# Kernel tuning notes

Measured on AMD Instinct MI355X. Metric: run time of the kernel, lower is better.

The kernel has to match this reference:

```python
import jax, jax.numpy as jnp
import numpy as np

B, L, D_MODEL, HEAD, DK = 4, 4096, 1024, 8, 128
ROUNDS, BUCKET = 4, 64
N_BUCKETS = L // BUCKET  # number of hash buckets AND number of chunks
NEG, SELF_PEN, EPS = -1e9, -1e5, 1e-5


def setup_inputs() -> dict:
    key = jax.random.key(0)
    ks = jax.random.split(key, 9)
    s = 0.02
    rot = jax.random.normal(ks[5], (DK, ROUNDS, N_BUCKETS // 2), dtype=jnp.float32)
    rot = rot / (jnp.linalg.norm(rot, axis=0, keepdims=True) + 1e-9)  # unit-norm rotations
    return {
        'x1': jax.random.normal(ks[0], (B, L, D_MODEL), jnp.float32),
        'x2': jax.random.normal(ks[1], (B, L, D_MODEL), jnp.float32),
        'wq': jax.random.normal(ks[2], (D_MODEL, D_MODEL), jnp.float32) * s,
        'bq': jnp.zeros((D_MODEL,), jnp.float32),
        'wv': jax.random.normal(ks[3], (D_MODEL, D_MODEL), jnp.float32) * s,
        'bv': jnp.zeros((D_MODEL,), jnp.float32),
        'wo': jax.random.normal(ks[4], (D_MODEL, D_MODEL), jnp.float32) * s,
        'bo': jnp.zeros((D_MODEL,), jnp.float32),
        'gamma': jnp.ones((D_MODEL,), jnp.float32),
        'beta': jnp.zeros((D_MODEL,), jnp.float32),
        'rot': rot,
        'mask': jnp.ones((B, L), jnp.bool_),
    }


def _look_back(t):
    # concat previous chunk (circular) with current chunk along intra-chunk axis
    prev = jnp.roll(t, 1, axis=3)
    return jnp.concatenate([prev, t], axis=4)


def _lsh_attention(x, mask, wq, bq, wv, bv, wo, bo, rot):
    # x: [B, L, D]; mask: [B, L] bool; rot: [DK, R, N_BUCKETS//2]
    q = (x @ wq + bq).reshape(B, L, HEAD, DK).transpose(0, 2, 1, 3)  # [B,H,L,dk]
    v = (x @ wv + bv).reshape(B, L, HEAD, DK).transpose(0, 2, 1, 3)
    # LSH hashing: argmax over [proj, -proj]
    proj = jnp.einsum('bhld,drn->bhrln', q, rot)  # [B,H,R,L,nb/2]
    hashes = jnp.argmax(jnp.concatenate([proj, -proj], axis=-1), axis=-1)  # [B,H,R,L]
    pos = jnp.arange(L)
    sort_idx = jnp.argsort(hashes * L + pos[None, None, None, :], axis=-1)  # stable sort by hash
    undo_idx = jnp.argsort(sort_idx, axis=-1)
    # gather q, v, positions, mask into hash-sorted order per round
    sq = jnp.take_along_axis(jnp.broadcast_to(q[:, :, None], (B, HEAD, ROUNDS, L, DK)), sort_idx[..., None], axis=3)
    sv = jnp.take_along_axis(jnp.broadcast_to(v[:, :, None], (B, HEAD, ROUNDS, L, DK)), sort_idx[..., None], axis=3)
    spos = jnp.take_along_axis(jnp.broadcast_to(pos, (B, HEAD, ROUNDS, L)), sort_idx, axis=3)
    smask = jnp.take_along_axis(jnp.broadcast_to(mask[:, None, None, :], (B, HEAD, ROUNDS, L)), sort_idx, axis=3)
    nc = L // BUCKET
    sq = sq.reshape(B, HEAD, ROUNDS, nc, BUCKET, DK)
    sv = sv.reshape(B, HEAD, ROUNDS, nc, BUCKET, DK)
    spos = spos.reshape(B, HEAD, ROUNDS, nc, BUCKET)
    smask = smask.reshape(B, HEAD, ROUNDS, nc, BUCKET)
    # shared-QK: keys are L2-normalized queries
    sk = sq / (jnp.linalg.norm(sq, axis=-1, keepdims=True) + 1e-9)
    k_lb, v_lb = _look_back(sk), _look_back(sv)          # [B,H,R,nc,2*BUCKET,dk]
    kpos, kmask = _look_back(spos[..., None]).squeeze(-1) if False else (_look_back(spos[..., None])[..., 0], _look_back(smask[..., None])[..., 0])
    scores = jnp.einsum('bhrcid,bhrcjd->bhrcij', sq, k_lb) / np.float32(np.sqrt(DK))
    qp = spos[..., :, None]
    kp = kpos[..., None, :]
    scores = jnp.where(kmask[..., None, :], scores, NEG)      # padding
    scores = jnp.where(kp > qp, NEG, scores)                  # causal
    scores = jnp.where(kp == qp, SELF_PEN, scores)            # discourage self-attention
    attn = jax.nn.softmax(scores, axis=-1)
    lse = jax.nn.logsumexp(scores, axis=-1)                   # [B,H,R,nc,BUCKET]
    o = jnp.einsum('bhrcij,bhrcjd->bhrcid', attn, v_lb).reshape(B, HEAD, ROUNDS, L, DK)
    lse = lse.reshape(B, HEAD, ROUNDS, L)
    # unsort back to original order
    o = jnp.take_along_axis(o, undo_idx[..., None], axis=3)
    lse = jnp.take_along_axis(lse, undo_idx, axis=3)
    # combine rounds with softmax over per-round logsumexp
    w = jax.nn.softmax(lse, axis=2)[..., None]                # [B,H,R,L,1]
    out = (w * o).sum(axis=2)                                 # [B,H,L,dk]
    out = out.transpose(0, 2, 1, 3).reshape(B, L, D_MODEL)
    return out @ wo + bo


def _layernorm(x, g, b):
    mu = jnp.mean(x, axis=-1, keepdims=True)
    var = jnp.mean((x - mu) ** 2, axis=-1, keepdims=True)
    return (x - mu) / jnp.sqrt(var + EPS) * g + b


def reference(x1, x2, wq, bq, wv, bv, wo, bo, gamma, beta, rot, mask):
    a = _lsh_attention(x2, mask, wq, bq, wv, bv, wo, bo, rot)
    y1 = x1 + _layernorm(a, gamma, beta)  # dropout is identity in eval
    return (y1, x2)
```

## Files before the change

kernel.cpp:

```cpp
#include <hip/hip_runtime.h>
#include <hip/hip_bf16.h>

#define B_ 4
#define L_ 4096
#define DM_ 1024
#define NH_ 8
#define DK_ 128
#define NR_ 4
#define NC_ 64
#define NEGV -1.0e9f
#define SELFP -1.0e5f
#define SQRTDK 11.313708498984761f
#define TAU 1.0e-3f
#define FCAP 524288
#define LOG2E 1.4426950408889634f
#define LN2 0.6931471805599453f

typedef __attribute__((ext_vector_type(8))) short short8;
typedef __attribute__((ext_vector_type(4))) float f32x4;

__device__ __forceinline__ unsigned short f2bf(float x) {
  unsigned u = __float_as_uint(x);
  u += 0x7FFFu + ((u >> 16) & 1u);
  return (unsigned short)(u >> 16);
}
__device__ __forceinline__ float bf2f(unsigned short h) {
  return __uint_as_float(((unsigned)h) << 16);
}
__device__ __forceinline__ float wlo(unsigned w) { return __uint_as_float(w << 16); }
__device__ __forceinline__ float whi(unsigned w) { return __uint_as_float(w & 0xFFFF0000u); }
__device__ __forceinline__ unsigned packbf(float a, float b) {
  unsigned r;
  asm("v_cvt_pk_bf16_f32 %0, %1, %2" : "=v"(r) : "v"(a), "v"(b));
  return r;
}
__device__ __forceinline__ float fexp2(float x) {
  float r;
  asm("v_exp_f32 %0, %1" : "=v"(r) : "v"(x));
  return r;
}
__device__ __forceinline__ float flog2(float x) {
  float r;
  asm("v_log_f32 %0, %1" : "=v"(r) : "v"(x));
  return r;
}
__device__ __forceinline__ unsigned packhi(float a, float b) {
  return (__float_as_uint(a) >> 16) | (__float_as_uint(b) & 0xFFFF0000u);
}
__device__ __forceinline__ float resid(float a) {
  return a - __uint_as_float(__float_as_uint(a) & 0xFFFF0000u);
}

__global__ __launch_bounds__(256) void cvtw_k(const float* __restrict__ W,
                                              unsigned short* __restrict__ Wt) {
  __shared__ float tile[64][65];
  const int t = threadIdx.x;
  const int bx = blockIdx.x & 15, by = blockIdx.x >> 4;
  const int c = t & 63, r4 = t >> 6;
#pragma unroll
  for (int i = 0; i < 16; i++) {
    int r = r4 * 16 + i;
    tile[r][c] = W[(size_t)(by * 64 + r) * DM_ + bx * 64 + c];
  }
  __syncthreads();
#pragma unroll
  for (int i = 0; i < 16; i++) {
    int r = r4 * 16 + i;
    Wt[(size_t)(bx * 64 + r) * DM_ + by * 64 + c] = f2bf(tile[c][r]);
  }
}

__global__ __launch_bounds__(256) void cvtw2_k(const float* __restrict__ W,
                                               unsigned short* __restrict__ Whi,
                                               unsigned short* __restrict__ Wlo) {
  __shared__ float tile[64][65];
  const int t = threadIdx.x;
  const int bx = blockIdx.x & 15, by = blockIdx.x >> 4;
  const int c = t & 63, r4 = t >> 6;
#pragma unroll
  for (int i = 0; i < 16; i++) {
    int r = r4 * 16 + i;
    tile[r][c] = W[(size_t)(by * 64 + r) * DM_ + bx * 64 + c];
  }
  __syncthreads();
#pragma unroll
  for (int i = 0; i < 16; i++) {
    int r = r4 * 16 + i;
    float v = tile[c][r];
    unsigned short h = f2bf(v);
    float lo = v - bf2f(h);
    size_t o = (size_t)(bx * 64 + r) * DM_ + by * 64 + c;
    Whi[o] = h;
    Wlo[o] = f2bf(lo);
  }
}

__global__ __launch_bounds__(256) void cvtrot_k(const float* __restrict__ rot,
                                                unsigned short* __restrict__ Rhi,
                                                unsigned short* __restrict__ Rlo) {
  int i = blockIdx.x * 256 + threadIdx.x;
  float v = rot[i];
  unsigned short h = f2bf(v);
  float lo = v - bf2f(h);
  int d = i >> 7, np = i & 127;
  Rhi[np * 128 + d] = h;
  Rlo[np * 128 + d] = f2bf(lo);
}

__global__ __launch_bounds__(256) void wproj_k(const float* __restrict__ W,
                                               const float* __restrict__ rot,
                                               float* __restrict__ Wp,
                                               int* __restrict__ cnt) {
  __shared__ float ws_[8][128];
  __shared__ float rs[128][33];
  const int t = threadIdx.x;
  const int hr = blockIdx.x >> 7;
  const int kc = blockIdx.x & 127;
  const int h = hr >> 2, r = hr & 3;
  if (blockIdx.x == 0 && t == 0) *cnt = 0;
  for (int i = t; i < 4096; i += 256) {
    int d = i >> 5, n = i & 31;
    rs[d][n] = rot[(size_t)d * 128 + r * 32 + n];
  }
  {
    int kk = t >> 5, dd = (t & 31) * 4;
    const float* wr = W + (size_t)(kc * 8 + kk) * DM_ + h * 128 + dd;
    float4 wv = *(const float4*)wr;
    ws_[kk][dd] = wv.x; ws_[kk][dd + 1] = wv.y;
    ws_[kk][dd + 2] = wv.z; ws_[kk][dd + 3] = wv.w;
  }
  __syncthreads();
  const int n = t & 31, kk = t >> 5;
  float s0 = 0.f, s1 = 0.f, s2 = 0.f, s3 = 0.f;
#pragma unroll
  for (int d = 0; d < 128; d += 4) {
    s0 = fmaf(ws_[kk][d], rs[d][n], s0);
    s1 = fmaf(ws_[kk][d + 1], rs[d + 1][n], s1);
    s2 = fmaf(ws_[kk][d + 2], rs[d + 2][n], s2);
    s3 = fmaf(ws_[kk][d + 3], rs[d + 3][n], s3);
  }
  Wp[((size_t)(h * 4 + r) * 32 + n) * 1024 + kc * 8 + kk] = (s0 + s1) + (s2 + s3);
}

__global__ __launch_bounds__(256) void gemm_qs(const unsigned short* __restrict__ Whi,
                                               const unsigned short* __restrict__ Wlo,
                                               const float* __restrict__ X,
                                               const float* __restrict__ bias,
                                               float* __restrict__ outF) {
  __shared__ __align__(16) unsigned short Ph[128 * 32];
  __shared__ __align__(16) unsigned short Pl[128 * 32];
  __shared__ __align__(16) unsigned short Qh[128 * 32];
  __shared__ __align__(16) unsigned short Ql[128 * 32];
  __shared__ float bias_s[128];
  const int t = threadIdx.x;
  const int bi = blockIdx.x;
  const int pb = (bi & 7) << 7;
  const int qb = (bi >> 3) << 7;
  if (t < 128) bias_s[t] = bias[pb + t];
  const int srow = t >> 1, shalf = t & 1;
  const unsigned short* Ph_p = Whi + (size_t)(pb + srow) * DM_ + shalf * 16;
  const unsigned short* Pl_p = Wlo + (size_t)(pb + srow) * DM_ + shalf * 16;
  const float* Xf = X + (size_t)(qb + srow) * DM_ + shalf * 16;
  const int lane = t & 63, wid = t >> 6;
  const int lm = lane & 15, quad = lane >> 4;
  const int prw = (wid & 1) << 6, qcw = (wid >> 1) << 6;
  const int sg = (quad ^ (lm & 3)) << 3;
  f32x4 acc[4][4];
#pragma unroll
  for (int i = 0; i < 4; i++)
#pragma unroll
    for (int j = 0; j < 4; j++) acc[i][j] = (f32x4){0.f, 0.f, 0.f, 0.f};
  uint4 phA, phB, plA, plB, qhA, qhB, qlA, qlB;
  {
    phA = *(const uint4*)(Ph_p);
    phB = *(const uint4*)(Ph_p + 8);
    plA = *(const uint4*)(Pl_p);
    plB = *(const uint4*)(Pl_p + 8);
    float4 f0 = *(const float4*)(Xf), f1 = *(const float4*)(Xf + 4);
    float4 f2 = *(const float4*)(Xf + 8), f3 = *(const float4*)(Xf + 12);
    qhA.x = packhi(f0.x, f0.y); qhA.y = packhi(f0.z, f0.w);
    qhA.z = packhi(f1.x, f1.y); qhA.w = packhi(f1.z, f1.w);
    qhB.x = packhi(f2.x, f2.y); qhB.y = packhi(f2.z, f2.w);
    qhB.z = packhi(f3.x, f3.y); qhB.w = packhi(f3.z, f3.w);
    qlA.x = packbf(resid(f0.x), resid(f0.y)); qlA.y = packbf(resid(f0.z), resid(f0.w));
    qlA.z = packbf(resid(f1.x), resid(f1.y)); qlA.w = packbf(resid(f1.z), resid(f1.w));
    qlB.x = packbf(resid(f2.x), resid(f2.y)); qlB.y = packbf(resid(f2.z), resid(f2.w));
    qlB.z = packbf(resid(f3.x), resid(f3.y)); qlB.w = packbf(resid(f3.z), resid(f3.w));
  }
  const int sw = srow & 3, g0 = shalf * 2;
  const int d0s = srow * 32 + ((g0 ^ sw) << 3);
  const int d1s = srow * 32 + (((g0 + 1) ^ sw) << 3);
  for (int kb = 0; kb < 32; ++kb) {
    __syncthreads();
    *(uint4*)&Ph[d0s] = phA; *(uint4*)&Ph[d1s] = phB;
    *(uint4*)&Pl[d0s] = plA; *(uint4*)&Pl[d1s] = plB;
    *(uint4*)&Qh[d0s] = qhA; *(uint4*)&Qh[d1s] = qhB;
    *(uint4*)&Ql[d0s] = qlA; *(uint4*)&Ql[d1s] = qlB;
    __syncthreads();
    if (kb < 31) {
      int ko = (kb + 1) * 32;
      phA = *(const uint4*)(Ph_p + ko);
      phB = *(const uint4*)(Ph_p + ko + 8);
      plA = *(const uint4*)(Pl_p + ko);
      plB = *(const uint4*)(Pl_p + ko + 8);
      const float* xp = Xf + ko;
      float4 f0 = *(const float4*)(xp), f1 = *(const float4*)(xp + 4);
      float4 f2 = *(const float4*)(xp + 8), f3 = *(const float4*)(xp + 12);
      qhA.x = packhi(f0.x, f0.y); qhA.y = packhi(f0.z, f0.w);
      qhA.z = packhi(f1.x, f1.y); qhA.w = packhi(f1.z, f1.w);
      qhB.x = packhi(f2.x, f2.y); qhB.y = packhi(f2.z, f2.w);
      qhB.z = packhi(f3.x, f3.y); qhB.w = packhi(f3.z, f3.w);
      qlA.x = packbf(resid(f0.x), resid(f0.y)); qlA.y = packbf(resid(f0.z), resid(f0.w));
      qlA.z = packbf(resid(f1.x), resid(f1.y)); qlA.w = packbf(resid(f1.z), resid(f1.w));
      qlB.x = packbf(resid(f2.x), resid(f2.y)); qlB.y = packbf(resid(f2.z), resid(f2.w));
      qlB.z = packbf(resid(f3.x), resid(f3.y)); qlB.w = packbf(resid(f3.z), resid(f3.w));
    }
    short8 ph[4], pl[4], qh[4], ql[4];
#pragma unroll
    for (int ti = 0; ti < 4; ti++) {
      int ro = (prw + ti * 16 + lm) * 32 + sg;
      ph[ti] = *(const short8*)&Ph[ro];
      pl[ti] = *(const short8*)&Pl[ro];
    }
#pragma unroll
    for (int tj = 0; tj < 4; tj++) {
      int ro = (qcw + tj * 16 + lm) * 32 + sg;
      qh[tj] = *(const short8*)&Qh[ro];
      ql[tj] = *(const short8*)&Ql[ro];
    }
#pragma unroll
    for (int ti = 0; ti < 4; ti++)
#pragma unroll
      for (int tj = 0; tj < 4; tj++) {
        f32x4 a = acc[ti][tj];
        a = __builtin_amdgcn_mfma_f32_16x16x32_bf16(ph[ti], qh[tj], a, 0, 0, 0);
        a = __builtin_amdgcn_mfma_f32_16x16x32_bf16(ph[ti], ql[tj], a, 0, 0, 0);
        a = __builtin_amdgcn_mfma_f32_16x16x32_bf16(pl[ti], qh[tj], a, 0, 0, 0);
        acc[ti][tj] = a;
      }
  }
  const int head = bi & 7;
#pragma unroll
  for (int tj = 0; tj < 4; tj++) {
    int mm = qb + qcw + tj * 16 + lm;
    int b = mm >> 12, l = mm & 4095;
    float* op = outF + ((size_t)(b * NH_ + head) * L_ + l) * DK_;
#pragma unroll
    for (int ti = 0; ti < 4; ti++) {
      int d0 = prw + ti * 16 + quad * 4;
      float4 w;
      w.x = acc[ti][tj][0] + bias_s[d0];
      w.y = acc[ti][tj][1] + bias_s[d0 + 1];
      w.z = acc[ti][tj][2] + bias_s[d0 + 2];
      w.w = acc[ti][tj][3] + bias_s[d0 + 3];
      *(float4*)(op + d0) = w;
    }
  }
}

template <int MODE>
__global__ __launch_bounds__(256) void gemm_bf(const unsigned short* __restrict__ Pm,
                                               const void* __restrict__ Qv,
                                               const float* __restrict__ bias,
                                               float* __restrict__ outF,
                                               unsigned int* __restrict__ outW) {
  __shared__ __align__(16) unsigned short Ps[128 * 32];
  __shared__ __align__(16) unsigned short Qs[128 * 32];
  __shared__ float bias_s[128];
  const int t = threadIdx.x;
  const int bi = blockIdx.x;
  const int pb = (MODE == 0) ? ((bi >> 3) << 7) : ((bi & 7) << 7);
  const int qb = (MODE == 0) ? ((bi & 7) << 7) : ((bi >> 3) << 7);
  if (t < 128) bias_s[t] = bias[((MODE == 0) ? qb : pb) + t];
  const int srow = t >> 1, shalf = t & 1;
  const unsigned short* Pp = Pm + (size_t)(pb + srow) * DM_ + shalf * 16;
  const float* Qf = (const float*)Qv + (size_t)(qb + srow) * DM_ + shalf * 16;
  const unsigned short* Qh = (const unsigned short*)Qv + (size_t)(qb + srow) * DM_ + shalf * 16;
  const int lane = t & 63, wid = t >> 6;
  const int lm = lane & 15, quad = lane >> 4;
  const int prw = (wid & 1) << 6, qcw = (wid >> 1) << 6;
  f32x4 acc[4][4];
#pragma unroll
  for (int i = 0; i < 4; i++)
#pragma unroll
    for (int j = 0; j < 4; j++) acc[i][j] = (f32x4){0.f, 0.f, 0.f, 0.f};
  uint4 pA, pB, qA, qB;
  {
    pA = *(const uint4*)(Pp);
    pB = *(const uint4*)(Pp + 8);
    if (MODE == 2) {
      float4 f0 = *(const float4*)(Qf), f1 = *(const float4*)(Qf + 4);
      float4 f2 = *(const float4*)(Qf + 8), f3 = *(const float4*)(Qf + 12);
      qA.x = packbf(f0.x, f0.y); qA.y = packbf(f0.z, f0.w);
      qA.z = packbf(f1.x, f1.y); qA.w = packbf(f1.z, f1.w);
      qB.x = packbf(f2.x, f2.y); qB.y = packbf(f2.z, f2.w);
      qB.z = packbf(f3.x, f3.y); qB.w = packbf(f3.z, f3.w);
    } else {
      qA = *(const uint4*)(Qh);
      qB = *(const uint4*)(Qh + 8);
    }
  }
  const int sdst = srow * 32 + shalf * 16;
  for (int kb = 0; kb < 32; ++kb) {
    __syncthreads();
    *(uint4*)&Ps[sdst] = pA;
    *(uint4*)&Ps[sdst + 8] = pB;
    *(uint4*)&Qs[sdst] = qA;
    *(uint4*)&Qs[sdst + 8] = qB;
    __syncthreads();
    if (kb < 31) {
      int ko = (kb + 1) * 32;
      pA = *(const uint4*)(Pp + ko);
      pB = *(const uint4*)(Pp + ko + 8);
      if (MODE == 2) {
        const float* qp = Qf + ko;
        float4 f0 = *(const float4*)(qp), f1 = *(const float4*)(qp + 4);
        float4 f2 = *(const float4*)(qp + 8), f3 = *(const float4*)(qp + 12);
        qA.x = packbf(f0.x, f0.y); qA.y = packbf(f0.z, f0.w);
        qA.z = packbf(f1.x, f1.y); qA.w = packbf(f1.z, f1.w);
        qB.x = packbf(f2.x, f2.y); qB.y = packbf(f2.z, f2.w);
        qB.z = packbf(f3.x, f3.y); qB.w = packbf(f3.z, f3.w);
      } else {
        qA = *(const uint4*)(Qh + ko);
        qB = *(const uint4*)(Qh + ko + 8);
      }
    }
    short8 pf[4], qf[4];
#pragma unroll
    for (int ti = 0; ti < 4; ti++)
      pf[ti] = *(const short8*)&Ps[(prw + ti * 16 + lm) * 32 + quad * 8];
#pragma unroll
    for (int tj = 0; tj < 4; tj++)
      qf[tj] = *(const short8*)&Qs[(qcw + tj * 16 + lm) * 32 + quad * 8];
#pragma unroll
    for (int ti = 0; ti < 4; ti++)
#pragma unroll
      for (int tj = 0; tj < 4; tj++)
        acc[ti][tj] = __builtin_amdgcn_mfma_f32_16x16x32_bf16(pf[ti], qf[tj], acc[ti][tj], 0, 0, 0);
  }
  if (MODE == 0) {
#pragma unroll
    for (int ti = 0; ti < 4; ti++) {
      int m = pb + prw + ti * 16 + quad * 4;
#pragma unroll
      for (int tj = 0; tj < 4; tj++) {
        int nn = qcw + tj * 16 + lm;
        float bn = bias_s[nn];
        float* op = outF + (size_t)m * DM_ + qb + nn;
#pragma unroll
        for (int r = 0; r < 4; r++) op[(size_t)r * DM_] = acc[ti][tj][r] + bn;
      }
    }
  } else {
    const int head = bi & 7;
#pragma unroll
    for (int tj = 0; tj < 4; tj++) {
      int mm = qb + qcw + tj * 16 + lm;
      int b = mm >> 12, l = mm & 4095;
#pragma unroll
      for (int ti = 0; ti < 4; ti++) {
        int d0 = prw + ti * 16 + quad * 4;
        uint2 ov;
        ov.x = packbf(acc[ti][tj][0] + bias_s[d0], acc[ti][tj][1] + bias_s[d0 + 1]);
        ov.y = packbf(acc[ti][tj][2] + bias_s[d0 + 2], acc[ti][tj][3] + bias_s[d0 + 3]);
        *(uint2*)(outW + ((size_t)(b * NH_ + head) * L_ + l) * 64 + (d0 >> 1)) = ov;
      }
    }
  }
}

#define HSTR 132
__global__ __launch_bounds__(256) void hashg_k(const unsigned short* __restrict__ Rhi,
                                               const unsigned short* __restrict__ Rlo,
                                               const float* __restrict__ q,
                                               unsigned char* __restrict__ hout,
                                               int* __restrict__ cnt,
                                               int* __restrict__ flags) {
  __shared__ __align__(16) char smraw[128 * HSTR * 4];
  unsigned short* Ph = (unsigned short*)smraw;
  unsigned short* Pl = Ph + 4096;
  unsigned short* Qh = Ph + 8192;
  unsigned short* Ql = Ph + 12288;
  float* S = (float*)smraw;
  const int t = threadIdx.x;
  const int bi = blockIdx.x;
  const int srow = t >> 1, shalf = t & 1;
  const unsigned short* Php = Rhi + srow * 128 + shalf * 16;
  const unsigned short* Plp = Rlo + srow * 128 + shalf * 16;
  const float* Qf = q + (size_t)(bi * 128 + srow) * DK_ + shalf * 16;
  const int lane = t & 63, wid = t >> 6;
  const int lm = lane & 15, quad = lane >> 4;
  const int prw = (wid & 1) << 6, qcw = (wid >> 1) << 6;
  const int sg = (quad ^ (lm & 3)) << 3;
  f32x4 acc[4][4];
#pragma unroll
  for (int i = 0; i < 4; i++)
#pragma unroll
    for (int j = 0; j < 4; j++) acc[i][j] = (f32x4){0.f, 0.f, 0.f, 0.f};
  const int sw = srow & 3, g0 = shalf * 2;
  const int d0s = srow * 32 + ((g0 ^ sw) << 3);
  const int d1s = srow * 32 + (((g0 + 1) ^ sw) << 3);
  for (int kb = 0; kb < 4; ++kb) {
    const int ko = kb * 32;
    uint4 phA = *(const uint4*)(Php + ko);
    uint4 phB = *(const uint4*)(Php + ko + 8);
    uint4 plA = *(const uint4*)(Plp + ko);
    uint4 plB = *(const uint4*)(Plp + ko + 8);
    const float* xp = Qf + ko;
    float4 f0 = *(const float4*)(xp), f1 = *(const float4*)(xp + 4);
    float4 f2 = *(const float4*)(xp + 8), f3 = *(const float4*)(xp + 12);
    uint4 qhA, qhB, qlA, qlB;
    qhA.x = packhi(f0.x, f0.y); qhA.y = packhi(f0.z, f0.w);
    qhA.z = packhi(f1.x, f1.y); qhA.w = packhi(f1.z, f1.w);
    qhB.x = packhi(f2.x, f2.y); qhB.y = packhi(f2.z, f2.w);
    qhB.z = packhi(f3.x, f3.y); qhB.w = packhi(f3.z, f3.w);
    qlA.x = packbf(resid(f0.x), resid(f0.y)); qlA.y = packbf(resid(f0.z), resid(f0.w));
    qlA.z = packbf(resid(f1.x), resid(f1.y)); qlA.w = packbf(resid(f1.z), resid(f1.w));
    qlB.x = packbf(resid(f2.x), resid(f2.y)); qlB.y = packbf(resid(f2.z), resid(f2.w));
    qlB.z = packbf(resid(f3.x), resid(f3.y)); qlB.w = packbf(resid(f3.z), resid(f3.w));
    __syncthreads();
    *(uint4*)&Ph[d0s] = phA; *(uint4*)&Ph[d1s] = phB;
    *(uint4*)&Pl[d0s] = plA; *(uint4*)&Pl[d1s] = plB;
    *(uint4*)&Qh[d0s] = qhA; *(uint4*)&Qh[d1s] = qhB;
    *(uint4*)&Ql[d0s] = qlA; *(uint4*)&Ql[d1s] = qlB;
    __syncthreads();
    short8 ph[4], pl[4], qh[4], ql[4];
#pragma unroll
    for (int ti = 0; ti < 4; ti++) {
      int ro = (prw + ti * 16 + lm) * 32 + sg;
      ph[ti] = *(const short8*)&Ph[ro];
      pl[ti] = *(const short8*)&Pl[ro];
    }
#pragma unroll
    for (int tj = 0; tj < 4; tj++) {
      int ro = (qcw + tj * 16 + lm) * 32 + sg;
      qh[tj] = *(const short8*)&Qh[ro];
      ql[tj] = *(const short8*)&Ql[ro];
    }
#pragma unroll
    for (int ti = 0; ti < 4; ti++)
#pragma unroll
      for (int tj = 0; tj < 4; tj++) {
        f32x4 a = acc[ti][tj];
        a = __builtin_amdgcn_mfma_f32_16x16x32_bf16(ph[ti], qh[tj], a, 0, 0, 0);
        a = __builtin_amdgcn_mfma_f32_16x16x32_bf16(ph[ti], ql[tj], a, 0, 0, 0);
        a = __builtin_amdgcn_mfma_f32_16x16x32_bf16(pl[ti], qh[tj], a, 0, 0, 0);
        acc[ti][tj] = a;
      }
  }
  __syncthreads();
#pragma unroll
  for (int ti = 0; ti < 4; ti++)
#pragma unroll
    for (int tj = 0; tj < 4; tj++) {
      int nn = qcw + tj * 16 + lm;
#pragma unroll
      for (int r = 0; r < 4; r++)
        S[(prw + ti * 16 + quad * 4 + r) * HSTR + nn] = acc[ti][tj][r];
    }
  __syncthreads();
#pragma unroll
  for (int pp = t; pp < 512; pp += 256) {
    int tok = pp & 127, r = pp >> 7;
    float best = -1.f, second = -1.f;
    int bidx = 0;
#pragma unroll
    for (int n = 0; n < 32; n++) {
      float v = S[(r * 32 + n) * HSTR + tok];
      float av = fabsf(v);
      int idx = (v >= 0.f) ? n : (n + 32);
      if (av > best) {
        second = best; best = av; bidx = idx;
      } else {
        if (av == best && idx < bidx) bidx = idx;
        second = fmaxf(second, av);
      }
    }
    int mm = bi * 128 + tok;
    int bh = mm >> 12, l = mm & 4095;
    hout[((size_t)(bh * NR_ + r)) * L_ + l] = (unsigned char)bidx;
    if (best - second < TAU) {
      int slot = atomicAdd(cnt, 1);
      if (slot < FCAP) flags[slot] = (((bh << 2) | r) << 12) | l;
    }
  }
}

__global__ __launch_bounds__(256) void fixup_k(const int* __restrict__ cnt,
                                               const int* __restrict__ flags,
                                               const float* __restrict__ X,
                                               const float* __restrict__ Wp,
                                               unsigned char* __restrict__ hout) {
  __shared__ float xs[1024];
  __shared__ float pv[32];
  int nflag = *cnt;
  if (nflag > FCAP) nflag = FCAP;
  const int t = threadIdx.x;
  for (int i = blockIdx.x; i < nflag; i += gridDim.x) {
    int f = flags[i];
    int l = f & 4095, r = (f >> 12) & 3, bh = f >> 14;
    int b = bh >> 3, h = bh & 7;
    __syncthreads();
    ((float4*)xs)[t] = ((const float4*)(X + ((size_t)b * L_ + l) * DM_))[t];
    __syncthreads();
    const int nn = t >> 3, kl = t & 7;
    const float* wrow = Wp + ((size_t)(h * 4 + r) * 32 + nn) * 1024 + kl * 4;
    float s = 0.f;
#pragma unroll 8
    for (int k0 = 0; k0 < 1024; k0 += 32) {
      float4 wv = *(const float4*)(wrow + k0);
      float4 xv = *(const float4*)(xs + k0 + kl * 4);
      s = fmaf(wv.x, xv.x, fmaf(wv.y, xv.y, fmaf(wv.z, xv.z, fmaf(wv.w, xv.w, s))));
    }
    s += __shfl_xor(s, 1);
    s += __shfl_xor(s, 2);
    s += __shfl_xor(s, 4);
    if (kl == 0) pv[nn] = s;
    __syncthreads();
    if (t == 0) {
      float bestv = -1.f;
      int besti = 0;
      for (int j = 0; j < 32; j++) {
        float p = pv[j];
        float ap = fabsf(p);
        int idx = (p >= 0.f) ? j : (j + 32);
        if (ap > bestv || (ap == bestv && idx < besti)) { bestv = ap; besti = idx; }
      }
      hout[((size_t)(bh * NR_ + r)) * L_ + l] = (unsigned char)besti;
    }
  }
}

__global__ __launch_bounds__(256) void sort_k(const unsigned char* __restrict__ hsh,
                                              int* __restrict__ sidx) {
  __shared__ unsigned char seg[256 * 64];
  __shared__ unsigned short grp[16 * 64];
  __shared__ int offs[64];
  __shared__ int tot[64];
  const int t = threadIdx.x;
  const int bhr = blockIdx.x;
  uint4 hv = ((const uint4*)(hsh + (size_t)bhr * L_))[t];
  unsigned hb[4] = {hv.x, hv.y, hv.z, hv.w};
  unsigned int* seg32 = (unsigned int*)seg;
#pragma unroll
  for (int i = 0; i < 16; i++) seg32[t * 16 + i] = 0;
  ((unsigned int*)grp)[t * 2] = 0;
  ((unsigned int*)grp)[t * 2 + 1] = 0;
  __syncthreads();
#pragma unroll
  for (int k = 0; k < 16; k++) {
    int h = (hb[k >> 2] >> ((k & 3) * 8)) & 0xFF;
    seg[t * 64 + h] = (unsigned char)(seg[t * 64 + h] + 1);
  }
  __syncthreads();
  {
    int h = t & 63;
    for (int g = (t >> 6); g < 16; g += 4) {
      int run = 0;
      for (int s = 0; s < 16; s++) {
        int idx = ((g << 4) + s) * 64 + h;
        int c = seg[idx];
        seg[idx] = (unsigned char)run;
        run += c;
      }
      grp[g * 64 + h] = (unsigned short)run;
    }
  }
  __syncthreads();
  if (t < 64) {
    int run = 0;
    for (int g = 0; g < 16; g++) {
      int c = grp[g * 64 + t];
      grp[g * 64 + t] = (unsigned short)run;
      run += c;
    }
    tot[t] = run;
  }
  __syncthreads();
  if (t == 0) {
    int run = 0;
    for (int h = 0; h < 64; h++) { offs[h] = run; run += tot[h]; }
  }
  __syncthreads();
  const int gbase = (t >> 4) * 64;
  int* outp = sidx + (size_t)bhr * L_;
#pragma unroll
  for (int k = 0; k < 16; k++) {
    int h = (hb[k >> 2] >> ((k & 3) * 8)) & 0xFF;
    int pos = offs[h] + grp[gbase + h] + seg[t * 64 + h];
    seg[t * 64 + h] = (unsigned char)(seg[t * 64 + h] + 1);
    outp[pos] = t * 16 + k;
  }
}

#define KSTR 136
__global__ __launch_bounds__(256) void attn_k(const float* __restrict__ q,
                                              const unsigned int* __restrict__ vwg,
                                              const int* __restrict__ sidx,
                                              float* __restrict__ lseG,
                                              unsigned int* __restrict__ oW) {
  __shared__ __align__(16) unsigned short R1[128 * KSTR];
  __shared__ __align__(16) unsigned short R2[64 * KSTR];
  __shared__ int idxs[128];
  const int t = threadIdx.x;
  const int c = blockIdx.x & 63;
  const int bhr = blockIdx.x >> 6;
  const int bh = bhr >> 2;
  const int pc = (c + 63) & 63;
  if (t < 128) {
    int sp = (t < 64) ? (pc * 64 + t) : (c * 64 + t - 64);
    idxs[t] = sidx[(size_t)bhr * L_ + sp];
  }
  __syncthreads();
  {
    const int row = t >> 1, half = t & 1;
    const float4* qp = (const float4*)(q + ((size_t)bh * L_ + idxs[row]) * DK_ + half * 64);
    float4 f[16];
    float ss = 0.f;
#pragma unroll
    for (int u = 0; u < 16; u++) {
      f[u] = qp[u];
      ss = fmaf(f[u].x, f[u].x, fmaf(f[u].y, f[u].y, fmaf(f[u].z, f[u].z, fmaf(f[u].w, f[u].w, ss))));
    }
    ss += __shfl_xor(ss, 1);
    float rn = 1.f / (sqrtf(ss) + 1e-9f);
    unsigned short* kr = R1 + row * KSTR + half * 64;
#pragma unroll
    for (int u = 0; u < 8; u++) {
      uint4 w4;
      w4.x = packbf(f[2 * u].x * rn, f[2 * u].y * rn);
      w4.y = packbf(f[2 * u].z * rn, f[2 * u].w * rn);
      w4.z = packbf(f[2 * u + 1].x * rn, f[2 * u + 1].y * rn);
      w4.w = packbf(f[2 * u + 1].z * rn, f[2 * u + 1].w * rn);
      *(uint4*)(kr + u * 8) = w4;
    }
    if (row >= 64) {
      unsigned short* qr = R2 + (row - 64) * KSTR + half * 64;
#pragma unroll
      for (int u = 0; u < 8; u++) {
        uint4 w4;
        w4.x = packbf(f[2 * u].x, f[2 * u].y);
        w4.y = packbf(f[2 * u].z, f[2 * u].w);
        w4.z = packbf(f[2 * u + 1].x, f[2 * u + 1].y);
        w4.w = packbf(f[2 * u + 1].z, f[2 * u + 1].w);
        *(uint4*)(qr + u * 8) = w4;
      }
    }
  }
  __syncthreads();
  const int lane = t & 63, wv = t >> 6;
  const int m0 = wv * 16;
  const int lm = lane & 15, quad = lane >> 4;
  f32x4 acc[8];
  {
    short8 af[4];
#pragma unroll
    for (int ks = 0; ks < 4; ks++)
      af[ks] = *(const short8*)(R2 + (m0 + lm) * KSTR + ks * 32 + quad * 8);
#pragma unroll
    for (int n = 0; n < 8; n++) {
      f32x4 a = {0.f, 0.f, 0.f, 0.f};
#pragma unroll
      for (int ks = 0; ks < 4; ks++) {
        short8 bf = *(const short8*)(R1 + (n * 16 + lm) * KSTR + ks * 32 + quad * 8);
        a = __builtin_amdgcn_mfma_f32_16x16x32_bf16(af[ks], bf, a, 0, 0, 0);
      }
      acc[n] = a;
    }
  }
  int qp4[4];
#pragma unroll
  for (int r = 0; r < 4; r++) qp4[r] = idxs[64 + m0 + quad * 4 + r];
#pragma unroll
  for (int n = 0; n < 8; n++) {
    int kp = idxs[n * 16 + lm];
#pragma unroll
    for (int r = 0; r < 4; r++) {
      float s = acc[n][r] * (1.f / SQRTDK);
      acc[n][r] = (kp > qp4[r]) ? NEGV : ((kp == qp4[r]) ? SELFP : s);
    }
  }
  uint4 vv[8];
  {
    const int key = t >> 1, half = t & 1;
    const uint4* vp = (const uint4*)(vwg + ((size_t)bh * L_ + idxs[key]) * 64 + half * 32);
#pragma unroll
    for (int u = 0; u < 8; u++) vv[u] = vp[u];
  }
  float mrow[4], sum4[4], inv4[4];
#pragma unroll
  for (int r = 0; r < 4; r++) {
    float mx = acc[0][r];
#pragma unroll
    for (int n = 1; n < 8; n++) mx = fmaxf(mx, acc[n][r]);
    mx = fmaxf(mx, __shfl_xor(mx, 1));
    mx = fmaxf(mx, __shfl_xor(mx, 2));
    mx = fmaxf(mx, __shfl_xor(mx, 4));
    mx = fmaxf(mx, __shfl_xor(mx, 8));
    mrow[r] = mx;
    sum4[r] = 0.f;
  }
#pragma unroll
  for (int n = 0; n < 8; n++) {
#pragma unroll
    for (int r = 0; r < 4; r++) {
      float e = fexp2((acc[n][r] - mrow[r]) * LOG2E);
      unsigned pk = packbf(e, e);
      R2[(m0 + quad * 4 + r) * KSTR + n * 16 + lm] = (unsigned short)pk;
      sum4[r] += wlo(pk);
    }
  }
#pragma unroll
  for (int r = 0; r < 4; r++) {
    float s = sum4[r];
    s += __shfl_xor(s, 1);
    s += __shfl_xor(s, 2);
    s += __shfl_xor(s, 4);
    s += __shfl_xor(s, 8);
    sum4[r] = s;
    inv4[r] = 1.f / s;
  }
  if (lm == 0) {
#pragma unroll
    for (int r = 0; r < 4; r++)
      lseG[(size_t)bhr * L_ + idxs[64 + m0 + quad * 4 + r]] = mrow[r] + flog2(sum4[r]) * LN2;
  }
  __syncthreads();
  {
    const int key = t >> 1, half = t & 1;
#pragma unroll
    for (int u = 0; u < 8; u++) {
      unsigned wd[4] = {vv[u].x, vv[u].y, vv[u].z, vv[u].w};
#pragma unroll
      for (int cc = 0; cc < 4; cc++) {
        int w = half * 32 + u * 4 + cc;
        R1[(2 * w) * KSTR + key] = (unsigned short)(wd[cc] & 0xFFFFu);
        R1[(2 * w + 1) * KSTR + key] = (unsigned short)(wd[cc] >> 16);
      }
    }
  }
  __syncthreads();
  f32x4 acc2[8];
  {
    short8 af[4];
#pragma unroll
    for (int ks = 0; ks < 4; ks++)
      af[ks] = *(const short8*)(R2 + (m0 + lm) * KSTR + ks * 32 + quad * 8);
#pragma unroll
    for (int n = 0; n < 8; n++) {
      f32x4 a = {0.f, 0.f, 0.f, 0.f};
#pragma unroll
      for (int ks = 0; ks < 4; ks++) {
        short8 bf = *(const short8*)(R1 + (n * 16 + lm) * KSTR + ks * 32 + quad * 8);
        a = __builtin_amdgcn_mfma_f32_16x16x32_bf16(af[ks], bf, a, 0, 0, 0);
      }
      acc2[n] = a;
    }
  }
#pragma unroll
  for (int n = 0; n < 8; n++) {
#pragma unroll
    for (int r = 0; r < 4; r++) {
      float o = acc2[n][r] * inv4[r];
      R2[(m0 + quad * 4 + r) * KSTR + n * 16 + lm] = (unsigned short)packbf(o, o);
    }
  }
  __syncthreads();
  {
    const int row = t >> 2, seg = t & 3;
    int l = idxs[64 + row];
    unsigned int* op = oW + ((size_t)bhr * L_ + l) * 64 + seg * 16;
    const unsigned short* rp = R2 + row * KSTR + seg * 32;
#pragma unroll
    for (int u = 0; u < 4; u++) *(uint4*)(op + u * 4) = *(const uint4*)(rp + u * 8);
  }
}

__global__ __launch_bounds__(256) void comb_k(const float* __restrict__ lse,
                                              const unsigned int* __restrict__ oW,
                                              unsigned int* __restrict__ aoutW) {
  size_t g = (size_t)blockIdx.x * 256 + threadIdx.x;
  int w = (int)(g & 63);
  int l = (int)((g >> 6) & 4095);
  int bh = (int)(g >> 18);
  float ls[4];
#pragma unroll
  for (int r = 0; r < 4; r++) ls[r] = lse[((size_t)(bh * 4 + r)) * L_ + l];
  float m = fmaxf(fmaxf(ls[0], ls[1]), fmaxf(ls[2], ls[3]));
  float wsum = 0.f, a0 = 0.f, a1 = 0.f;
#pragma unroll
  for (int r = 0; r < 4; r++) {
    float e = fexp2((ls[r] - m) * LOG2E);
    wsum += e;
    unsigned ow = oW[(((size_t)(bh * 4 + r)) * L_ + l) * 64 + w];
    a0 = fmaf(e, wlo(ow), a0);
    a1 = fmaf(e, whi(ow), a1);
  }
  float inv = 1.f / wsum;
  int b = bh >> 3, h = bh & 7;
  aoutW[((size_t)b * L_ + l) * 512 + h * 64 + w] = packbf(a0 * inv, a1 * inv);
}

__global__ __launch_bounds__(256) void ln_k(const float* __restrict__ a,
                                            const float* __restrict__ x1,
                                            const float* __restrict__ x2,
                                            const float* __restrict__ gamma,
                                            const float* __restrict__ beta,
                                            float* __restrict__ out) {
  __shared__ float red[256];
  __shared__ float red2[256];
  const int t = threadIdx.x;
  const size_t row = blockIdx.x;
  float4 av = *(const float4*)(a + row * DM_ + t * 4);
  red[t] = av.x + av.y + av.z + av.w;
  red2[t] = av.x * av.x + av.y * av.y + av.z * av.z + av.w * av.w;
  __syncthreads();
  for (int off = 128; off > 0; off >>= 1) {
    if (t < off) { red[t] += red[t + off]; red2[t] += red2[t + off]; }
    __syncthreads();
  }
  float mu = red[0] * (1.f / 1024.f);
  float var = red2[0] * (1.f / 1024.f) - mu * mu;
  float rstd = rsqrtf(var + 1e-5f);
  float4 g4 = *(const float4*)(gamma + t * 4);
  float4 b4 = *(const float4*)(beta + t * 4);
  float4 x14 = *(const float4*)(x1 + row * DM_ + t * 4);
  float4 o4;
  o4.x = x14.x + (av.x - mu) * rstd * g4.x + b4.x;
  o4.y = x14.y + (av.y - mu) * rstd * g4.y + b4.y;
  o4.z = x14.z + (av.z - mu) * rstd * g4.z + b4.z;
  o4.w = x14.w + (av.w - mu) * rstd * g4.w + b4.w;
  *(float4*)(out + row * DM_ + t * 4) = o4;
  float4 x24 = *(const float4*)(x2 + row * DM_ + t * 4);
  *(float4*)(out + (size_t)B_ * L_ * DM_ + row * DM_ + t * 4) = x24;
}

extern "C" void kernel_launch(void* const* d_in, const int* in_sizes, int n_in,
                              void* d_out, int out_size, void* d_ws, size_t ws_size,
                              hipStream_t stream) {
  const float* x1 = (const float*)d_in[0];
  const float* x2 = (const float*)d_in[1];
  const float* wq = (const float*)d_in[2];
  const float* bq = (const float*)d_in[3];
  const float* wv = (const float*)d_in[4];
  const float* bv = (const float*)d_in[5];
  const float* wo = (const float*)d_in[6];
  const float* bo = (const float*)d_in[7];
  const float* gamma = (const float*)d_in[8];
  const float* beta = (const float*)d_in[9];
  const float* rot = (const float*)d_in[10];

  char* ws = (char*)d_ws;
  float* qbuf = (float*)ws;
  unsigned int* vbuf = (unsigned int*)(ws + 67108864);
  unsigned char* hbuf = (unsigned char*)(ws + 100663296);
  int* sbuf = (int*)(ws + 101187584);
  float* lbuf = (float*)(ws + 103284736);
  unsigned int* obuf = (unsigned int*)(ws + 105381888);
  float* abuf = (float*)(ws + 105381888);
  unsigned short* wtqh = (unsigned short*)(ws + 105381888);
  unsigned short* wtql = (unsigned short*)(ws + 107479040);
  float* wproj = (float*)(ws + 109576192);
  int* flags = (int*)(ws + 113770496);
  int* cntb = (int*)(ws + 115867648);
  unsigned short* rthi = (unsigned short*)(ws + 115871744);
  unsigned short* rtlo = (unsigned short*)(ws + 115904512);
  unsigned short* wtv = (unsigned short*)(ws + 172490752);
  unsigned short* wto = (unsigned short*)(ws + 174587904);
  unsigned int* aoutW = (unsigned int*)ws;
  float* out = (float*)d_out;

  dim3 blk(256);
  cvtw2_k<<<dim3(256), blk, 0, stream>>>(wq, wtqh, wtql);
  wproj_k<<<dim3(4096), blk, 0, stream>>>(wq, rot, wproj, cntb);
  cvtrot_k<<<dim3(64), blk, 0, stream>>>(rot, rthi, rtlo);
  gemm_qs<<<dim3(1024), blk, 0, stream>>>(wtqh, wtql, x2, bq, qbuf);
  cvtw_k<<<dim3(256), blk, 0, stream>>>(wv, wtv);
  gemm_bf<2><<<dim3(1024), blk, 0, stream>>>(wtv, (const void*)x2, bv, nullptr, vbuf);
  hashg_k<<<dim3(1024), blk, 0, stream>>>(rthi, rtlo, qbuf, hbuf, cntb, flags);
  fixup_k<<<dim3(1024), blk, 0, stream>>>(cntb, flags, x2, wproj, hbuf);
  sort_k<<<dim3(128), blk, 0, stream>>>(hbuf, sbuf);
  attn_k<<<dim3(8192), blk, 0, stream>>>(qbuf, vbuf, sbuf, lbuf, obuf);
  comb_k<<<dim3(32768), blk, 0, stream>>>(lbuf, obuf, aoutW);
  cvtw_k<<<dim3(256), blk, 0, stream>>>(wo, wto);
  gemm_bf<0><<<dim3(1024), blk, 0, stream>>>((const unsigned short*)aoutW, (const void*)wto,
                                             bo, abuf, nullptr);
  ln_k<<<dim3(16384), blk, 0, stream>>>(abuf, x1, x2, gamma, beta, out);
}
```

Before: 802.7 us.

## Pre-split x2 into bf16 hi/lo and stage GEMM tiles via global_load_lds

```diff
diff --git a/kernel.cpp b/kernel.cpp
--- a/kernel.cpp
+++ b/kernel.cpp
@@ -19,6 +19,13 @@
 typedef __attribute__((ext_vector_type(8))) short short8;
 typedef __attribute__((ext_vector_type(4))) float f32x4;
 
+#define GLD(gp, lp)                                                                   \
+  __builtin_amdgcn_global_load_lds((const __attribute__((address_space(1))) unsigned  \
+                                        int*)(gp),                                    \
+                                   (__attribute__((address_space(3))) unsigned int*)( \
+                                       lp),                                           \
+                                   16, 0, 0)
+
 __device__ __forceinline__ unsigned short f2bf(float x) {
   unsigned u = __float_as_uint(x);
   u += 0x7FFFu + ((u >> 16) & 1u);
@@ -49,6 +56,18 @@
 }
 __device__ __forceinline__ float resid(float a) {
   return a - __uint_as_float(__float_as_uint(a) & 0xFFFF0000u);
+}
+
+__global__ __launch_bounds__(256) void xsplit_k(const float* __restrict__ X,
+                                                unsigned int* __restrict__ Xhi,
+                                                unsigned int* __restrict__ Xlo) {
+  size_t i = ((size_t)blockIdx.x * 256 + threadIdx.x) * 2;
+  float4 v = *(const float4*)(X + i * 2);
+  unsigned h0 = packbf(v.x, v.y), h1 = packbf(v.z, v.w);
+  unsigned l0 = packbf(v.x - wlo(h0), v.y - whi(h0));
+  unsigned l1 = packbf(v.z - wlo(h1), v.w - whi(h1));
+  *(uint2*)(Xhi + i) = make_uint2(h0, h1);
+  *(uint2*)(Xlo + i) = make_uint2(l0, l1);
 }
 
 __global__ __launch_bounds__(256) void cvtw_k(const float* __restrict__ W,
@@ -144,7 +163,8 @@
 
 __global__ __launch_bounds__(256) void gemm_qs(const unsigned short* __restrict__ Whi,
                                                const unsigned short* __restrict__ Wlo,
-                                               const float* __restrict__ X,
+                                               const unsigned short* __restrict__ Xhi,
+                                               const unsigned short* __restrict__ Xlo,
                                                const float* __restrict__ bias,
                                                float* __restrict__ outF) {
   __shared__ __align__(16) unsigned short Ph[128 * 32];
@@ -157,74 +177,43 @@
   const int pb = (bi & 7) << 7;
   const int qb = (bi >> 3) << 7;
   if (t < 128) bias_s[t] = bias[pb + t];
-  const int srow = t >> 1, shalf = t & 1;
-  const unsigned short* Ph_p = Whi + (size_t)(pb + srow) * DM_ + shalf * 16;
-  const unsigned short* Pl_p = Wlo + (size_t)(pb + srow) * DM_ + shalf * 16;
-  const float* Xf = X + (size_t)(qb + srow) * DM_ + shalf * 16;
   const int lane = t & 63, wid = t >> 6;
   const int lm = lane & 15, quad = lane >> 4;
   const int prw = (wid & 1) << 6, qcw = (wid >> 1) << 6;
-  const int sg = (quad ^ (lm & 3)) << 3;
+  const int jA = wid * 2, jB = jA + 1;
+  const int rA = (jA << 4) + (lane >> 2), rB = (jB << 4) + (lane >> 2);
+  const int qg = (lane & 3) << 3;
+  const unsigned short* phA = Whi + (size_t)(pb + rA) * DM_ + qg;
+  const unsigned short* phB = Whi + (size_t)(pb + rB) * DM_ + qg;
+  const unsigned short* plA = Wlo + (size_t)(pb + rA) * DM_ + qg;
+  const unsigned short* plB = Wlo + (size_t)(pb + rB) * DM_ + qg;
+  const unsigned short* qhA = Xhi + (size_t)(qb + rA) * DM_ + qg;
+  const unsigned short* qhB = Xhi + (size_t)(qb + rB) * DM_ + qg;
+  const unsigned short* qlA = Xlo + (size_t)(qb + rA) * DM_ + qg;
+  const unsigned short* qlB = Xlo + (size_t)(qb + rB) * DM_ + qg;
   f32x4 acc[4][4];
 #pragma unroll
   for (int i = 0; i < 4; i++)
 #pragma unroll
     for (int j = 0; j < 4; j++) acc[i][j] = (f32x4){0.f, 0.f, 0.f, 0.f};
-  uint4 phA, phB, plA, plB, qhA, qhB, qlA, qlB;
-  {
-    phA = *(const uint4*)(Ph_p);
-    phB = *(const uint4*)(Ph_p + 8);
-    plA = *(const uint4*)(Pl_p);
-    plB = *(const uint4*)(Pl_p + 8);
-    float4 f0 = *(const float4*)(Xf), f1 = *(const float4*)(Xf + 4);
-    float4 f2 = *(const float4*)(Xf + 8), f3 = *(const float4*)(Xf + 12);
-    qhA.x = packhi(f0.x, f0.y); qhA.y = packhi(f0.z, f0.w);
-    qhA.z = packhi(f1.x, f1.y); qhA.w = packhi(f1.z, f1.w);
-    qhB.x = packhi(f2.x, f2.y); qhB.y = packhi(f2.z, f2.w);
-    qhB.z = packhi(f3.x, f3.y); qhB.w = packhi(f3.z, f3.w);
-    qlA.x = packbf(resid(f0.x), resid(f0.y)); qlA.y = packbf(resid(f0.z), resid(f0.w));
-    qlA.z = packbf(resid(f1.x), resid(f1.y)); qlA.w = packbf(resid(f1.z), resid(f1.w));
-    qlB.x = packbf(resid(f2.x), resid(f2.y)); qlB.y = packbf(resid(f2.z), resid(f2.w));
-    qlB.z = packbf(resid(f3.x), resid(f3.y)); qlB.w = packbf(resid(f3.z), resid(f3.w));
-  }
-  const int sw = srow & 3, g0 = shalf * 2;
-  const int d0s = srow * 32 + ((g0 ^ sw) << 3);
-  const int d1s = srow * 32 + (((g0 + 1) ^ sw) << 3);
   for (int kb = 0; kb < 32; ++kb) {
-    __syncthreads();
-    *(uint4*)&Ph[d0s] = phA; *(uint4*)&Ph[d1s] = phB;
-    *(uint4*)&Pl[d0s] = plA; *(uint4*)&Pl[d1s] = plB;
-    *(uint4*)&Qh[d0s] = qhA; *(uint4*)&Qh[d1s] = qhB;
-    *(uint4*)&Ql[d0s] = qlA; *(uint4*)&Ql[d1s] = qlB;
-    __syncthreads();
-    if (kb < 31) {
-      int ko = (kb + 1) * 32;
-      phA = *(const uint4*)(Ph_p + ko);
-      phB = *(const uint4*)(Ph_p + ko + 8);
-      plA = *(const uint4*)(Pl_p + ko);
-      plB = *(const uint4*)(Pl_p + ko + 8);
-      const float* xp = Xf + ko;
-      float4 f0 = *(const float4*)(xp), f1 = *(const float4*)(xp + 4);
-      float4 f2 = *(const float4*)(xp + 8), f3 = *(const float4*)(xp + 12);
-      qhA.x = packhi(f0.x, f0.y); qhA.y = packhi(f0.z, f0.w);
-      qhA.z = packhi(f1.x, f1.y); qhA.w = packhi(f1.z, f1.w);
-      qhB.x = packhi(f2.x, f2.y); qhB.y = packhi(f2.z, f2.w);
-      qhB.z = packhi(f3.x, f3.y); qhB.w = packhi(f3.z, f3.w);
-      qlA.x = packbf(resid(f0.x), resid(f0.y)); qlA.y = packbf(resid(f0.z), resid(f0.w));
-      qlA.z = packbf(resid(f1.x), resid(f1.y)); qlA.w = packbf(resid(f1.z), resid(f1.w));
-      qlB.x = packbf(resid(f2.x), resid(f2.y)); qlB.y = packbf(resid(f2.z), resid(f2.w));
-      qlB.z = packbf(resid(f3.x), resid(f3.y)); qlB.w = packbf(resid(f3.z), resid(f3.w));
-    }
+    const int ko = kb * 32;
+    __syncthreads();
+    GLD(phA + ko, Ph + jA * 512); GLD(phB + ko, Ph + jB * 512);
+    GLD(plA + ko, Pl + jA * 512); GLD(plB + ko, Pl + jB * 512);
+    GLD(qhA + ko, Qh + jA * 512); GLD(qhB + ko, Qh + jB * 512);
+    GLD(qlA + ko, Ql + jA * 512); GLD(qlB + ko, Ql + jB * 512);
+    __syncthreads();
     short8 ph[4], pl[4], qh[4], ql[4];
 #pragma unroll
     for (int ti = 0; ti < 4; ti++) {
-      int ro = (prw + ti * 16 + lm) * 32 + sg;
+      int ro = (prw + ti * 16 + lm) * 32 + quad * 8;
       ph[ti] = *(const short8*)&Ph[ro];
       pl[ti] = *(const short8*)&Pl[ro];
     }
 #pragma unroll
     for (int tj = 0; tj < 4; tj++) {
-      int ro = (qcw + tj * 16 + lm) * 32 + sg;
+      int ro = (qcw + tj * 16 + lm) * 32 + quad * 8;
       qh[tj] = *(const short8*)&Qh[ro];
       ql[tj] = *(const short8*)&Ql[ro];
     }
@@ -260,7 +249,7 @@
 
 template <int MODE>
 __global__ __launch_bounds__(256) void gemm_bf(const unsigned short* __restrict__ Pm,
-                                               const void* __restrict__ Qv,
+                                               const unsigned short* __restrict__ Qm,
                                                const float* __restrict__ bias,
                                                float* __restrict__ outF,
                                                unsigned int* __restrict__ outW) {
@@ -272,59 +261,27 @@
   const int pb = (MODE == 0) ? ((bi >> 3) << 7) : ((bi & 7) << 7);
   const int qb = (MODE == 0) ? ((bi & 7) << 7) : ((bi >> 3) << 7);
   if (t < 128) bias_s[t] = bias[((MODE == 0) ? qb : pb) + t];
-  const int srow = t >> 1, shalf = t & 1;
-  const unsigned short* Pp = Pm + (size_t)(pb + srow) * DM_ + shalf * 16;
-  const float* Qf = (const float*)Qv + (size_t)(qb + srow) * DM_ + shalf * 16;
-  const unsigned short* Qh = (const unsigned short*)Qv + (size_t)(qb + srow) * DM_ + shalf * 16;
   const int lane = t & 63, wid = t >> 6;
   const int lm = lane & 15, quad = lane >> 4;
   const int prw = (wid & 1) << 6, qcw = (wid >> 1) << 6;
+  const int jA = wid * 2, jB = jA + 1;
+  const int rA = (jA << 4) + (lane >> 2), rB = (jB << 4) + (lane >> 2);
+  const int qg = (lane & 3) << 3;
+  const unsigned short* pA_ = Pm + (size_t)(pb + rA) * DM_ + qg;
+  const unsigned short* pB_ = Pm + (size_t)(pb + rB) * DM_ + qg;
+  const unsigned short* qA_ = Qm + (size_t)(qb + rA) * DM_ + qg;
+  const unsigned short* qB_ = Qm + (size_t)(qb + rB) * DM_ + qg;
   f32x4 acc[4][4];
 #pragma unroll
   for (int i = 0; i < 4; i++)
 #pragma unroll
     for (int j = 0; j < 4; j++) acc[i][j] = (f32x4){0.f, 0.f, 0.f, 0.f};
-  uint4 pA, pB, qA, qB;
-  {
-    pA = *(const uint4*)(Pp);
-    pB = *(const uint4*)(Pp + 8);
-    if (MODE == 2) {
-      float4 f0 = *(const float4*)(Qf), f1 = *(const float4*)(Qf + 4);
-      float4 f2 = *(const float4*)(Qf + 8), f3 = *(const float4*)(Qf + 12);
-      qA.x = packbf(f0.x, f0.y); qA.y = packbf(f0.z, f0.w);
-      qA.z = packbf(f1.x, f1.y); qA.w = packbf(f1.z, f1.w);
-      qB.x = packbf(f2.x, f2.y); qB.y = packbf(f2.z, f2.w);
-      qB.z = packbf(f3.x, f3.y); qB.w = packbf(f3.z, f3.w);
-    } else {
-      qA = *(const uint4*)(Qh);
-      qB = *(const uint4*)(Qh + 8);
-    }
-  }
-  const int sdst = srow * 32 + shalf * 16;
   for (int kb = 0; kb < 32; ++kb) {
-    __syncthreads();
-    *(uint4*)&Ps[sdst] = pA;
-    *(uint4*)&Ps[sdst + 8] = pB;
-    *(uint4*)&Qs[sdst] = qA;
-    *(uint4*)&Qs[sdst + 8] = qB;
-    __syncthreads();
-    if (kb < 31) {
-      int ko = (kb + 1) * 32;
-      pA = *(const uint4*)(Pp + ko);
-      pB = *(const uint4*)(Pp + ko + 8);
-      if (MODE == 2) {
-        const float* qp = Qf + ko;
-        float4 f0 = *(const float4*)(qp), f1 = *(const float4*)(qp + 4);
-        float4 f2 = *(const float4*)(qp + 8), f3 = *(const float4*)(qp + 12);
-        qA.x = packbf(f0.x, f0.y); qA.y = packbf(f0.z, f0.w);
-        qA.z = packbf(f1.x, f1.y); qA.w = packbf(f1.z, f1.w);
-        qB.x = packbf(f2.x, f2.y); qB.y = packbf(f2.z, f2.w);
-        qB.z = packbf(f3.x, f3.y); qB.w = packbf(f3.z, f3.w);
-      } else {
-        qA = *(const uint4*)(Qh + ko);
-        qB = *(const uint4*)(Qh + ko + 8);
-      }
-    }
+    const int ko = kb * 32;
+    __syncthreads();
+    GLD(pA_ + ko, Ps + jA * 512); GLD(pB_ + ko, Ps + jB * 512);
+    GLD(qA_ + ko, Qs + jA * 512); GLD(qB_ + ko, Qs + jB * 512);
+    __syncthreads();
     short8 pf[4], qf[4];
 #pragma unroll
     for (int ti = 0; ti < 4; ti++)
@@ -603,8 +560,10 @@
   __shared__ __align__(16) unsigned short R2[64 * KSTR];
   __shared__ int idxs[128];
   const int t = threadIdx.x;
-  const int c = blockIdx.x & 63;
-  const int bhr = blockIdx.x >> 6;
+  const int bid0 = blockIdx.x;
+  const int wg = ((bid0 & 7) << 10) | (bid0 >> 3);
+  const int c = wg & 63;
+  const int bhr = wg >> 6;
   const int bh = bhr >> 2;
   const int pc = (c + 63) & 63;
   if (t < 128) {
@@ -865,25 +824,30 @@
   int* cntb = (int*)(ws + 115867648);
   unsigned short* rthi = (unsigned short*)(ws + 115871744);
   unsigned short* rtlo = (unsigned short*)(ws + 115904512);
-  unsigned short* wtv = (unsigned short*)(ws + 172490752);
-  unsigned short* wto = (unsigned short*)(ws + 174587904);
+  unsigned int* xhiW = (unsigned int*)(ws + 117440512);
+  unsigned int* xloW = (unsigned int*)(ws + 150994944);
+  unsigned short* wtv = (unsigned short*)(ws + 184549376);
+  unsigned short* wto = (unsigned short*)(ws + 186646528);
   unsigned int* aoutW = (unsigned int*)ws;
   float* out = (float*)d_out;
 
   dim3 blk(256);
+  xsplit_k<<<dim3(16384), blk, 0, stream>>>(x2, xhiW, xloW);
   cvtw2_k<<<dim3(256), blk, 0, stream>>>(wq, wtqh, wtql);
   wproj_k<<<dim3(4096), blk, 0, stream>>>(wq, rot, wproj, cntb);
   cvtrot_k<<<dim3(64), blk, 0, stream>>>(rot, rthi, rtlo);
-  gemm_qs<<<dim3(1024), blk, 0, stream>>>(wtqh, wtql, x2, bq, qbuf);
+  gemm_qs<<<dim3(1024), blk, 0, stream>>>(wtqh, wtql, (const unsigned short*)xhiW,
+                                          (const unsigned short*)xloW, bq, qbuf);
   cvtw_k<<<dim3(256), blk, 0, stream>>>(wv, wtv);
-  gemm_bf<2><<<dim3(1024), blk, 0, stream>>>(wtv, (const void*)x2, bv, nullptr, vbuf);
+  gemm_bf<2><<<dim3(1024), blk, 0, stream>>>(wtv, (const unsigned short*)xhiW, bv,
+                                             nullptr, vbuf);
   hashg_k<<<dim3(1024), blk, 0, stream>>>(rthi, rtlo, qbuf, hbuf, cntb, flags);
   fixup_k<<<dim3(1024), blk, 0, stream>>>(cntb, flags, x2, wproj, hbuf);
   sort_k<<<dim3(128), blk, 0, stream>>>(hbuf, sbuf);
   attn_k<<<dim3(8192), blk, 0, stream>>>(qbuf, vbuf, sbuf, lbuf, obuf);
   comb_k<<<dim3(32768), blk, 0, stream>>>(lbuf, obuf, aoutW);
   cvtw_k<<<dim3(256), blk, 0, stream>>>(wo, wto);
-  gemm_bf<0><<<dim3(1024), blk, 0, stream>>>((const unsigned short*)aoutW, (const void*)wto,
-                                             bo, abuf, nullptr);
+  gemm_bf<0><<<dim3(1024), blk, 0, stream>>>((const unsigned short*)aoutW, wto, bo,
+                                             abuf, nullptr);
   ln_k<<<dim3(16384), blk, 0, stream>>>(abuf, x1, x2, gamma, beta, out);
 }
```

Result: faster. 746.5 us (-7.0%).
